# Kernel optimization log

Measured on AMD Instinct MI355X. Metric: run time of the kernel, lower is better.

The kernel has to match this reference:

```python
import jax, jax.numpy as jnp
import numpy as np

HEADS = 16
EMBED = 1024
D_K = EMBED // HEADS


def setup_inputs() -> dict:
    key = jax.random.key(0)
    ks = jax.random.split(key, 11)
    B, S, E = 4, 2048, EMBED
    sc = 0.02
    return {
        "query": jax.random.normal(ks[0], (B, S, E), jnp.float32),
        "key_": jax.random.normal(ks[1], (B, S, E), jnp.float32),
        "value": jax.random.normal(ks[2], (B, S, E), jnp.float32),
        "Wq": jax.random.normal(ks[3], (E, E), jnp.float32) * sc,
        "bq": jnp.zeros((E,), jnp.float32),
        "Wk": jax.random.normal(ks[4], (E, E), jnp.float32) * sc,
        "bk": jnp.zeros((E,), jnp.float32),
        "Wv": jax.random.normal(ks[5], (E, E), jnp.float32) * sc,
        "bv": jnp.zeros((E,), jnp.float32),
        "Wo": jax.random.normal(ks[6], (E, D_K), jnp.float32) * sc,  # out: Linear(heads*d_k -> d_k)
        "bo": jnp.zeros((D_K,), jnp.float32),
    }


def reference(query, key_, value, Wq, bq, Wk, bk, Wv, bv, Wo, bo):
    B, S, E = query.shape
    H, Dk = HEADS, D_K
    # QKV projections
    q = query @ Wq + bq          # (B,S,E)
    k = key_ @ Wk + bk
    v = value @ Wv + bv
    # split heads -> (B,H,S,Dk)
    q = q.reshape(B, S, H, Dk).transpose(0, 2, 1, 3)
    k = k.reshape(B, S, H, Dk).transpose(0, 2, 1, 3)
    v = v.reshape(B, S, H, Dk).transpose(0, 2, 1, 3)
    # attention: softmax(QK^T / sqrt(d_k)) V
    scores = jnp.einsum("bhqd,bhkd->bhqk", q, k) / jnp.sqrt(jnp.asarray(Dk, q.dtype))
    attn = jax.nn.softmax(scores, axis=-1)
    ctx = jnp.einsum("bhqk,bhkd->bhqd", attn, v)
    ctx = ctx.transpose(0, 2, 1, 3).reshape(B, S, E)
    # output projection (E -> d_k, as in source)
    return ctx @ Wo + bo
```

## Files before the change

kernel.cpp:

```cpp
#include <hip/hip_runtime.h>
#include <hip/hip_bf16.h>
#include <cstdint>
#include <cstddef>

#define DEVI static __device__ __forceinline__

typedef unsigned short u16;
typedef unsigned int u32;
typedef __bf16 bf16_t;
typedef __bf16 bf16x8 __attribute__((ext_vector_type(8)));
typedef float f32x4 __attribute__((ext_vector_type(4)));
typedef float f32x16 __attribute__((ext_vector_type(16)));

union U16x8 { uint4 u; bf16x8 v; };
union PU { u32 w[4]; bf16x8 v; };

#define QSCALE 0.1803368801111204f

DEVI void gload_lds16(const void* g, void* l) {
  __builtin_amdgcn_global_load_lds((const __attribute__((address_space(1))) void*)g,
                                   (__attribute__((address_space(3))) void*)l, 16, 0, 0);
}
DEVI void wait_vmcnt0() { asm volatile("s_waitcnt vmcnt(0)" ::: "memory"); }

DEVI u32 cvt_pk_bf16(float lo, float hi) {
  u32 r;
  asm("v_cvt_pk_bf16_f32 %0, %1, %2" : "=v"(r) : "v"(lo), "v"(hi));
  return r;
}

DEVI void permswap(u32& a, u32& b) {
  asm("v_permlane32_swap_b32 %0, %1" : "+v"(a), "+v"(b));
}

DEVI f32x16 mfma32(bf16x8 a, bf16x8 b, f32x16 c) {
  return __builtin_amdgcn_mfma_f32_32x32x16_bf16(a, b, c, 0, 0, 0);
}

DEVI bf16x8 lds_frag(const char* base, int row, int koff, int swz) {
  U16x8 u;
  u.u = *(const uint4*)(base + row * 128 + (koff ^ swz));
  return u.v;
}

__global__ __launch_bounds__(256) void k_transpose_convert(
    const float* __restrict__ src, bf16_t* __restrict__ dst, int R, int C, float scale) {
  int tiles_c = C >> 6;
  int tc = blockIdx.x % tiles_c;
  int tr = blockIdx.x / tiles_c;
  int r0 = tr << 6, c0 = tc << 6;
  __shared__ u16 tile[64][65];
  int t = threadIdx.x;
  #pragma unroll
  for (int p = 0; p < 4; ++p) {
    int idx = t + p * 256;
    int i = idx >> 4, j4 = (idx & 15) * 4;
    float4 f = *(const float4*)(src + (size_t)(r0 + i) * C + c0 + j4);
    tile[i][j4 + 0] = __builtin_bit_cast(u16, (bf16_t)(f.x * scale));
    tile[i][j4 + 1] = __builtin_bit_cast(u16, (bf16_t)(f.y * scale));
    tile[i][j4 + 2] = __builtin_bit_cast(u16, (bf16_t)(f.z * scale));
    tile[i][j4 + 3] = __builtin_bit_cast(u16, (bf16_t)(f.w * scale));
  }
  __syncthreads();
  #pragma unroll
  for (int p = 0; p < 2; ++p) {
    int idx = t + p * 256;
    int j = idx >> 3, i0 = (idx & 7) * 8;
    u16 us[8];
    #pragma unroll
    for (int e = 0; e < 8; ++e) us[e] = tile[i0 + e][j];
    uint4 o;
    o.x = (u32)us[0] | ((u32)us[1] << 16);
    o.y = (u32)us[2] | ((u32)us[3] << 16);
    o.z = (u32)us[4] | ((u32)us[5] << 16);
    o.w = (u32)us[6] | ((u32)us[7] << 16);
    *(uint4*)((u16*)dst + (size_t)(c0 + j) * R + r0 + i0) = o;
  }
}

__global__ __launch_bounds__(256) void k_proj_gemm(
    const float* __restrict__ Aq, const float* __restrict__ Ak, const float* __restrict__ Av,
    const bf16_t* __restrict__ WqT, const bf16_t* __restrict__ WkT, const bf16_t* __restrict__ WvT,
    const float* __restrict__ bq, const float* __restrict__ bk, const float* __restrict__ bv,
    bf16_t* __restrict__ qh, bf16_t* __restrict__ kh, bf16_t* __restrict__ vh) {
  int bx = blockIdx.x;
  int which = bx >> 9;
  int tt = bx & 511;
  int tile_m = tt & 63;
  int tile_n = tt >> 6;
  const float* A    = which == 0 ? Aq : which == 1 ? Ak : Av;
  const bf16_t* WT  = which == 0 ? WqT : which == 1 ? WkT : WvT;
  const float* bias = which == 0 ? bq : which == 1 ? bk : bv;
  const float bscale = which == 0 ? QSCALE : 1.0f;
  bf16_t* dst       = which == 0 ? qh : which == 1 ? kh : vh;

  const int t = threadIdx.x;
  const int l = t & 63;
  const int w = t >> 6;
  const int wm = w >> 1, wn = w & 1;
  const int c = l & 15, g = l >> 4;
  const int row0 = tile_m << 7;
  const int n0 = tile_n << 7;

  __shared__ __align__(16) char As[128 * 64 * 2];
  __shared__ __align__(16) char Bs[128 * 64 * 2];

  f32x4 acc[4][4];
  #pragma unroll
  for (int i = 0; i < 4; ++i)
    #pragma unroll
    for (int j = 0; j < 4; ++j) acc[i][j] = (f32x4){0.f, 0.f, 0.f, 0.f};

  const int arow_b = t >> 4, ac4 = t & 15;
  const int aswz = arow_b & 7;
  const float* agbase = A + (size_t)(row0 + arow_b) * 1024 + ac4 * 4;
  char* aldst = As + arow_b * 128 + (((ac4 >> 1) ^ aswz) << 4) + (ac4 & 1) * 8;

  for (int kt = 0; kt < 16; ++kt) {
    __syncthreads();
    {
      const float* ap = agbase + kt * 64;
      #pragma unroll
      for (int p = 0; p < 8; ++p) {
        float4 f = *(const float4*)(ap + (size_t)p * 16384);
        uint2 o;
        o.x = cvt_pk_bf16(f.x, f.y);
        o.y = cvt_pk_bf16(f.z, f.w);
        *(uint2*)(aldst + p * 2048) = o;
      }
    }
    #pragma unroll
    for (int cc = 0; cc < 4; ++cc) {
      int slot = w * 256 + cc * 64 + l;
      int row = slot >> 3, chs = slot & 7;
      const bf16_t* src = WT + (size_t)(n0 + row) * 1024 + kt * 64 + ((chs ^ (row & 7)) << 3);
      gload_lds16(src, Bs + (w * 256 + cc * 64) * 16);
    }
    wait_vmcnt0();
    __syncthreads();
    #pragma unroll
    for (int kk = 0; kk < 2; ++kk) {
      bf16x8 af[4], bfr[4];
      #pragma unroll
      for (int mi = 0; mi < 4; ++mi) {
        int row = wm * 64 + mi * 16 + c;
        U16x8 u; u.u = *(const uint4*)(As + row * 128 + ((kk * 64 + g * 16) ^ ((c & 7) << 4)));
        af[mi] = u.v;
      }
      #pragma unroll
      for (int ni = 0; ni < 4; ++ni) {
        int row = wn * 64 + ni * 16 + c;
        U16x8 u; u.u = *(const uint4*)(Bs + row * 128 + ((kk * 64 + g * 16) ^ ((c & 7) << 4)));
        bfr[ni] = u.v;
      }
      #pragma unroll
      for (int mi = 0; mi < 4; ++mi)
        #pragma unroll
        for (int ni = 0; ni < 4; ++ni)
          acc[mi][ni] = __builtin_amdgcn_mfma_f32_16x16x32_bf16(af[mi], bfr[ni], acc[mi][ni], 0, 0, 0);
    }
  }
  u16* dd = (u16*)dst;
  #pragma unroll
  for (int ni = 0; ni < 4; ++ni) {
    int col = n0 + wn * 64 + ni * 16 + c;
    float bb = bias[col] * bscale;
    int h = col >> 6, d = col & 63;
    #pragma unroll
    for (int mi = 0; mi < 4; ++mi) {
      #pragma unroll
      for (int r = 0; r < 4; ++r) {
        int rowg = row0 + wm * 64 + mi * 16 + g * 4 + r;
        int b = rowg >> 11, s = rowg & 2047;
        float vv = acc[mi][ni][r] + bb;
        size_t idx = (((size_t)b * 16 + h) * 2048 + s) * 64 + d;
        dd[idx] = __builtin_bit_cast(u16, (bf16_t)vv);
      }
    }
  }
}

__global__ __launch_bounds__(256) void k_transpose_v(
    const bf16_t* __restrict__ vh, bf16_t* __restrict__ vT) {
  int bh = blockIdx.x >> 5, st = blockIdx.x & 31;
  int s0 = st << 6;
  __shared__ __align__(16) u16 tile[64][72];
  int t = threadIdx.x;
  const u16* src = (const u16*)vh + ((size_t)bh * 2048 + s0) * 64;
  #pragma unroll
  for (int p = 0; p < 2; ++p) {
    int idx = t + p * 256;
    int s = idx >> 3, d0 = (idx & 7) * 8;
    uint4 v = *(const uint4*)(src + s * 64 + d0);
    *(uint4*)(&tile[s][d0]) = v;
  }
  __syncthreads();
  u16* dst = (u16*)vT + (size_t)bh * 64 * 2048 + s0;
  #pragma unroll
  for (int p = 0; p < 2; ++p) {
    int idx = t + p * 256;
    int d = idx >> 3, s1 = (idx & 7) * 8;
    u16 us[8];
    #pragma unroll
    for (int e = 0; e < 8; ++e) us[e] = tile[s1 + e][d];
    uint4 o;
    o.x = (u32)us[0] | ((u32)us[1] << 16);
    o.y = (u32)us[2] | ((u32)us[3] << 16);
    o.z = (u32)us[4] | ((u32)us[5] << 16);
    o.w = (u32)us[6] | ((u32)us[7] << 16);
    *(uint4*)(dst + (size_t)d * 2048 + s1) = o;
  }
}

__global__ __launch_bounds__(256, 4) void k_attn(
    const bf16_t* __restrict__ qh, const bf16_t* __restrict__ kh,
    const bf16_t* __restrict__ vT, bf16_t* __restrict__ ctx) {
  const int bid = blockIdx.x;
  const int bx = ((bid & 7) << 7) | (bid >> 3);
  const int bh = bx >> 4;
  const int qt = bx & 15;
  const int q0 = qt << 7;
  const int t = threadIdx.x, l = t & 63, w = t >> 6;
  const int q = l & 31;
  const int hi = l >> 5;
  const int swz = (q & 7) << 4;

  __shared__ __align__(16) char Ks[2][64 * 128];
  __shared__ __align__(16) char Vs[2][64 * 128];
  __shared__ __align__(16) float Dn[4][32];

  const u16* qrow = (const u16*)qh + ((size_t)bh * 2048 + q0 + w * 32 + q) * 64;
  bf16x8 qf0, qf1, qf2, qf3;
  {
    U16x8 u;
    u.u = *(const uint4*)(qrow + 0 * 16 + hi * 8); qf0 = u.v;
    u.u = *(const uint4*)(qrow + 1 * 16 + hi * 8); qf1 = u.v;
    u.u = *(const uint4*)(qrow + 2 * 16 + hi * 8); qf2 = u.v;
    u.u = *(const uint4*)(qrow + 3 * 16 + hi * 8); qf3 = u.v;
  }

  const f32x16 z16 = {0.f,0.f,0.f,0.f, 0.f,0.f,0.f,0.f, 0.f,0.f,0.f,0.f, 0.f,0.f,0.f,0.f};
  f32x16 oc0 = z16, oc1 = z16;
  float l_run = 0.f;

  const u16* kbh = (const u16*)kh + (size_t)bh * 2048 * 64;
  const u16* vbh = (const u16*)vT + (size_t)bh * 64 * 2048;

  auto stage = [&](int kvi, int buf) {
    int kbase = kvi << 6;
    #pragma unroll
    for (int cc = 0; cc < 2; ++cc) {
      int slot = w * 128 + cc * 64 + l;
      int row = slot >> 3, chs = slot & 7;
      gload_lds16(kbh + (size_t)(kbase + row) * 64 + ((chs ^ (row & 7)) << 3),
                  Ks[buf] + (w * 128 + cc * 64) * 16);
      gload_lds16(vbh + (size_t)row * 2048 + kbase + ((chs ^ (row & 7)) << 3),
                  Vs[buf] + (w * 128 + cc * 64) * 16);
    }
  };

  stage(0, 0);
  wait_vmcnt0();
  __syncthreads();

  for (int kv = 0; kv < 32; ++kv) {
    const int cur = kv & 1;
    if (kv < 31) stage(kv + 1, cur ^ 1);
    const char* Kc = Ks[cur];
    const char* Vc = Vs[cur];

    #pragma unroll
    for (int tt = 0; tt < 2; ++tt) {
      const int arow = tt * 32 + q;
      f32x16 st = z16;
      __builtin_amdgcn_s_setprio(1);
      st = mfma32(lds_frag(Kc, arow, 0 * 32 + hi * 16, swz), qf0, st);
      st = mfma32(lds_frag(Kc, arow, 1 * 32 + hi * 16, swz), qf1, st);
      st = mfma32(lds_frag(Kc, arow, 2 * 32 + hi * 16, swz), qf2, st);
      st = mfma32(lds_frag(Kc, arow, 3 * 32 + hi * 16, swz), qf3, st);
      __builtin_amdgcn_s_setprio(0);

      float e[16];
      #pragma unroll
      for (int i = 0; i < 16; ++i) {
        e[i] = __builtin_amdgcn_exp2f(st[i]);
        l_run += e[i];
      }

      #pragma unroll
      for (int cc = 0; cc < 2; ++cc) {
        u32 a  = cvt_pk_bf16(e[8 * cc + 0], e[8 * cc + 1]);
        u32 b  = cvt_pk_bf16(e[8 * cc + 4], e[8 * cc + 5]);
        u32 c2 = cvt_pk_bf16(e[8 * cc + 2], e[8 * cc + 3]);
        u32 d  = cvt_pk_bf16(e[8 * cc + 6], e[8 * cc + 7]);
        permswap(a, b);
        permswap(c2, d);
        PU pu;
        pu.w[0] = a; pu.w[1] = c2; pu.w[2] = b; pu.w[3] = d;
        const int ks = tt * 2 + cc;
        __builtin_amdgcn_s_setprio(1);
        oc0 = mfma32(pu.v, lds_frag(Vc, q,      ks * 32 + hi * 16, swz), oc0);
        oc1 = mfma32(pu.v, lds_frag(Vc, 32 + q, ks * 32 + hi * 16, swz), oc1);
        __builtin_amdgcn_s_setprio(0);
      }
    }
    wait_vmcnt0();
    __syncthreads();
  }

  l_run += __shfl_xor(l_run, 32);
  Dn[w][q] = 1.f / l_run;
  __syncthreads();

  const int b = bh >> 4, hh = bh & 15;
  u16* cb = (u16*)ctx;
  #pragma unroll
  for (int qd = 0; qd < 4; ++qd) {
    float4 dv = *(const float4*)&Dn[w][qd * 8 + hi * 4];
    #pragma unroll
    for (int r = 0; r < 4; ++r) {
      float inv = (&dv.x)[r];
      int qrow_g = q0 + w * 32 + qd * 8 + hi * 4 + r;
      size_t base = ((size_t)b * 2048 + qrow_g) * 1024 + hh * 64;
      float v0 = oc0[qd * 4 + r] * inv;
      float v1 = oc1[qd * 4 + r] * inv;
      cb[base + q]      = __builtin_bit_cast(u16, (bf16_t)v0);
      cb[base + 32 + q] = __builtin_bit_cast(u16, (bf16_t)v1);
    }
  }
}

__global__ __launch_bounds__(256) void k_out_gemm(
    const bf16_t* __restrict__ ctx, const bf16_t* __restrict__ WoT,
    const float* __restrict__ bo, float* __restrict__ out) {
  int tile_m = blockIdx.x;
  const int t = threadIdx.x, l = t & 63, w = t >> 6;
  const int wm = w >> 1, wn = w & 1;
  const int c = l & 15, g = l >> 4;
  const int row0 = tile_m << 7;

  __shared__ __align__(16) char As[128 * 64 * 2];
  __shared__ __align__(16) char Bs[64 * 64 * 2];

  f32x4 acc[4][2];
  #pragma unroll
  for (int i = 0; i < 4; ++i)
    #pragma unroll
    for (int j = 0; j < 2; ++j) acc[i][j] = (f32x4){0.f, 0.f, 0.f, 0.f};

  for (int kt = 0; kt < 16; ++kt) {
    __syncthreads();
    #pragma unroll
    for (int cc = 0; cc < 4; ++cc) {
      int slot = w * 256 + cc * 64 + l;
      int row = slot >> 3, chs = slot & 7;
      const bf16_t* src = ctx + (size_t)(row0 + row) * 1024 + kt * 64 + ((chs ^ (row & 7)) << 3);
      gload_lds16(src, As + (w * 256 + cc * 64) * 16);
    }
    #pragma unroll
    for (int cc = 0; cc < 2; ++cc) {
      int slot = w * 128 + cc * 64 + l;
      int row = slot >> 3, chs = slot & 7;
      const bf16_t* src = WoT + (size_t)row * 1024 + kt * 64 + ((chs ^ (row & 7)) << 3);
      gload_lds16(src, Bs + (w * 128 + cc * 64) * 16);
    }
    wait_vmcnt0();
    __syncthreads();
    #pragma unroll
    for (int kk = 0; kk < 2; ++kk) {
      bf16x8 af[4], bfr[2];
      #pragma unroll
      for (int mi = 0; mi < 4; ++mi) {
        int row = wm * 64 + mi * 16 + c;
        U16x8 u; u.u = *(const uint4*)(As + row * 128 + ((kk * 64 + g * 16) ^ ((c & 7) << 4)));
        af[mi] = u.v;
      }
      #pragma unroll
      for (int ni = 0; ni < 2; ++ni) {
        int row = wn * 32 + ni * 16 + c;
        U16x8 u; u.u = *(const uint4*)(Bs + row * 128 + ((kk * 64 + g * 16) ^ ((c & 7) << 4)));
        bfr[ni] = u.v;
      }
      #pragma unroll
      for (int mi = 0; mi < 4; ++mi)
        #pragma unroll
        for (int ni = 0; ni < 2; ++ni)
          acc[mi][ni] = __builtin_amdgcn_mfma_f32_16x16x32_bf16(af[mi], bfr[ni], acc[mi][ni], 0, 0, 0);
    }
  }
  #pragma unroll
  for (int ni = 0; ni < 2; ++ni) {
    int col = wn * 32 + ni * 16 + c;
    float bb = bo[col];
    #pragma unroll
    for (int mi = 0; mi < 4; ++mi) {
      #pragma unroll
      for (int r = 0; r < 4; ++r) {
        int rowg = row0 + wm * 64 + mi * 16 + g * 4 + r;
        out[(size_t)rowg * 64 + col] = acc[mi][ni][r] + bb;
      }
    }
  }
}

extern "C" void kernel_launch(void* const* d_in, const int* in_sizes, int n_in,
                              void* d_out, int out_size, void* d_ws, size_t ws_size,
                              hipStream_t stream) {
  (void)in_sizes; (void)n_in; (void)out_size; (void)ws_size;
  const float* query = (const float*)d_in[0];
  const float* key_  = (const float*)d_in[1];
  const float* value = (const float*)d_in[2];
  const float* Wq = (const float*)d_in[3];
  const float* bq = (const float*)d_in[4];
  const float* Wk = (const float*)d_in[5];
  const float* bk = (const float*)d_in[6];
  const float* Wv = (const float*)d_in[7];
  const float* bv = (const float*)d_in[8];
  const float* Wo = (const float*)d_in[9];
  const float* bo = (const float*)d_in[10];
  float* out = (float*)d_out;

  char* ws = (char*)d_ws;
  bf16_t* WqT = (bf16_t*)(ws + (size_t)0);
  bf16_t* WkT = (bf16_t*)(ws + ((size_t)2 << 20));
  bf16_t* WvT = (bf16_t*)(ws + ((size_t)4 << 20));
  bf16_t* WoT = (bf16_t*)(ws + ((size_t)6 << 20));
  bf16_t* qhd = (bf16_t*)(ws + ((size_t)8 << 20));
  bf16_t* khd = (bf16_t*)(ws + ((size_t)24 << 20));
  bf16_t* vhd = (bf16_t*)(ws + ((size_t)40 << 20));
  bf16_t* vT  = (bf16_t*)(ws + ((size_t)56 << 20));
  bf16_t* ctx = (bf16_t*)(ws + ((size_t)72 << 20));

  k_transpose_convert<<<256, 256, 0, stream>>>(Wq, WqT, 1024, 1024, QSCALE);
  k_transpose_convert<<<256, 256, 0, stream>>>(Wk, WkT, 1024, 1024, 1.0f);
  k_transpose_convert<<<256, 256, 0, stream>>>(Wv, WvT, 1024, 1024, 1.0f);
  k_transpose_convert<<<16, 256, 0, stream>>>(Wo, WoT, 1024, 64, 1.0f);

  k_proj_gemm<<<1536, 256, 0, stream>>>(query, key_, value, WqT, WkT, WvT,
                                        bq, bk, bv, qhd, khd, vhd);
  k_transpose_v<<<2048, 256, 0, stream>>>(vhd, vT);
  k_attn<<<1024, 256, 0, stream>>>(qhd, khd, vT, ctx);
  k_out_gemm<<<64, 256, 0, stream>>>(ctx, WoT, bo, out);
}
```

Baseline: 208.8 us.

## Register-prefetch next K tile in projection GEMM and remap tiles per XCD

The projection GEMM now loads the next K-slice of A and B into registers while the current slice is computed, replacing the synchronous global-to-LDS load plus wait each iteration. The B operand switches from direct global_load_lds to register staging. Block indices are also remapped so consecutive blocks on the same XCD share M tiles, which should improve L2 reuse. This roughly doubles the register footprint for staged tiles and could reduce occupancy.

```diff
diff --git a/kernel.cpp b/kernel.cpp
--- a/kernel.cpp
+++ b/kernel.cpp
@@ -83,11 +83,12 @@
     const bf16_t* __restrict__ WqT, const bf16_t* __restrict__ WkT, const bf16_t* __restrict__ WvT,
     const float* __restrict__ bq, const float* __restrict__ bk, const float* __restrict__ bv,
     bf16_t* __restrict__ qh, bf16_t* __restrict__ kh, bf16_t* __restrict__ vh) {
-  int bx = blockIdx.x;
-  int which = bx >> 9;
-  int tt = bx & 511;
-  int tile_m = tt & 63;
-  int tile_n = tt >> 6;
+  const int bid = blockIdx.x;
+  const int which = bid >> 9;
+  const int b9 = bid & 511;
+  const int xcd = b9 & 7, j = b9 >> 3;
+  const int tile_m = xcd * 8 + (j >> 3);
+  const int tile_n = j & 7;
   const float* A    = which == 0 ? Aq : which == 1 ? Ak : Av;
   const bf16_t* WT  = which == 0 ? WqT : which == 1 ? WkT : WvT;
   const float* bias = which == 0 ? bq : which == 1 ? bk : bv;
@@ -109,35 +110,43 @@
   #pragma unroll
   for (int i = 0; i < 4; ++i)
     #pragma unroll
-    for (int j = 0; j < 4; ++j) acc[i][j] = (f32x4){0.f, 0.f, 0.f, 0.f};
+    for (int jj = 0; jj < 4; ++jj) acc[i][jj] = (f32x4){0.f, 0.f, 0.f, 0.f};
 
   const int arow_b = t >> 4, ac4 = t & 15;
-  const int aswz = arow_b & 7;
   const float* agbase = A + (size_t)(row0 + arow_b) * 1024 + ac4 * 4;
-  char* aldst = As + arow_b * 128 + (((ac4 >> 1) ^ aswz) << 4) + (ac4 & 1) * 8;
-
-  for (int kt = 0; kt < 16; ++kt) {
-    __syncthreads();
-    {
-      const float* ap = agbase + kt * 64;
-      #pragma unroll
-      for (int p = 0; p < 8; ++p) {
-        float4 f = *(const float4*)(ap + (size_t)p * 16384);
-        uint2 o;
-        o.x = cvt_pk_bf16(f.x, f.y);
-        o.y = cvt_pk_bf16(f.z, f.w);
-        *(uint2*)(aldst + p * 2048) = o;
-      }
-    }
-    #pragma unroll
-    for (int cc = 0; cc < 4; ++cc) {
-      int slot = w * 256 + cc * 64 + l;
-      int row = slot >> 3, chs = slot & 7;
-      const bf16_t* src = WT + (size_t)(n0 + row) * 1024 + kt * 64 + ((chs ^ (row & 7)) << 3);
-      gload_lds16(src, Bs + (w * 256 + cc * 64) * 16);
-    }
-    wait_vmcnt0();
-    __syncthreads();
+  char* aldst = As + arow_b * 128 + (((ac4 >> 1) ^ (arow_b & 7)) << 4) + (ac4 & 1) * 8;
+
+  const int brow_b = t >> 3, bchs = t & 7;
+  const u16* bgbase = (const u16*)WT + (size_t)(n0 + brow_b) * 1024 + bchs * 8;
+  char* bldst = Bs + brow_b * 128 + ((bchs ^ (brow_b & 7)) << 4);
+
+  float4 fa0[8], fa1[8];
+  uint4 fb0[4], fb1[4];
+
+  auto loadA = [&](int kt, float4* f) {
+    const float* ap = agbase + kt * 64;
+    #pragma unroll
+    for (int p = 0; p < 8; ++p) f[p] = *(const float4*)(ap + (size_t)p * 16384);
+  };
+  auto loadB = [&](int kt, uint4* u) {
+    const u16* bp = bgbase + kt * 64;
+    #pragma unroll
+    for (int p = 0; p < 4; ++p) u[p] = *(const uint4*)(bp + (size_t)p * 32768);
+  };
+  auto storeA = [&](const float4* f) {
+    #pragma unroll
+    for (int p = 0; p < 8; ++p) {
+      uint2 o;
+      o.x = cvt_pk_bf16(f[p].x, f[p].y);
+      o.y = cvt_pk_bf16(f[p].z, f[p].w);
+      *(uint2*)(aldst + p * 2048) = o;
+    }
+  };
+  auto storeB = [&](const uint4* u) {
+    #pragma unroll
+    for (int p = 0; p < 4; ++p) *(uint4*)(bldst + p * 4096) = u[p];
+  };
+  auto compute = [&]() {
     #pragma unroll
     for (int kk = 0; kk < 2; ++kk) {
       bf16x8 af[4], bfr[4];
@@ -159,7 +168,22 @@
         for (int ni = 0; ni < 4; ++ni)
           acc[mi][ni] = __builtin_amdgcn_mfma_f32_16x16x32_bf16(af[mi], bfr[ni], acc[mi][ni], 0, 0, 0);
     }
-  }
+  };
+
+  loadA(0, fa0); loadB(0, fb0);
+  for (int i = 0; i < 8; ++i) {
+    __syncthreads();
+    storeA(fa0); storeB(fb0);
+    loadA(2 * i + 1, fa1); loadB(2 * i + 1, fb1);
+    __syncthreads();
+    compute();
+    __syncthreads();
+    storeA(fa1); storeB(fb1);
+    if (i < 7) { loadA(2 * i + 2, fa0); loadB(2 * i + 2, fb0); }
+    __syncthreads();
+    compute();
+  }
+
   u16* dd = (u16*)dst;
   #pragma unroll
   for (int ni = 0; ni < 4; ++ni) {
```

Result: slower. 286.7 us (+37.3%).

## Prefetch next K-tile into registers to overlap global loads with MFMA

Applied to the files above, without the earlier changes.

Restructures the QKV projection GEMM main loop so that the A (fp32) and B (bf16 weight) tiles for the next K step are loaded into registers while the current tile's MFMAs run, then converted and stored to LDS after a barrier. The weight tile now goes through registers instead of the direct global-to-LDS load path. This hides global memory latency behind compute, at the cost of more live registers (around 48 extra VGPRs for the prefetch buffers), which may lower occupancy.

```diff
diff --git a/kernel.cpp b/kernel.cpp
--- a/kernel.cpp
+++ b/kernel.cpp
@@ -83,11 +83,11 @@
     const bf16_t* __restrict__ WqT, const bf16_t* __restrict__ WkT, const bf16_t* __restrict__ WvT,
     const float* __restrict__ bq, const float* __restrict__ bk, const float* __restrict__ bv,
     bf16_t* __restrict__ qh, bf16_t* __restrict__ kh, bf16_t* __restrict__ vh) {
-  int bx = blockIdx.x;
-  int which = bx >> 9;
-  int tt = bx & 511;
-  int tile_m = tt & 63;
-  int tile_n = tt >> 6;
+  const int bx = blockIdx.x;
+  const int which = bx >> 9;
+  const int tt = bx & 511;
+  const int tile_m = tt & 63;
+  const int tile_n = tt >> 6;
   const float* A    = which == 0 ? Aq : which == 1 ? Ak : Av;
   const bf16_t* WT  = which == 0 ? WqT : which == 1 ? WkT : WvT;
   const float* bias = which == 0 ? bq : which == 1 ? bk : bv;
@@ -112,32 +112,40 @@
     for (int j = 0; j < 4; ++j) acc[i][j] = (f32x4){0.f, 0.f, 0.f, 0.f};
 
   const int arow_b = t >> 4, ac4 = t & 15;
-  const int aswz = arow_b & 7;
   const float* agbase = A + (size_t)(row0 + arow_b) * 1024 + ac4 * 4;
-  char* aldst = As + arow_b * 128 + (((ac4 >> 1) ^ aswz) << 4) + (ac4 & 1) * 8;
+  char* aldst = As + arow_b * 128 + (((ac4 >> 1) ^ (arow_b & 7)) << 4) + (ac4 & 1) * 8;
+
+  const int brow_b = t >> 3, bchs = t & 7;
+  const u16* bgbase = (const u16*)WT + (size_t)(n0 + brow_b) * 1024 + bchs * 8;
+  char* bldst = Bs + brow_b * 128 + ((bchs ^ (brow_b & 7)) << 4);
+
+  float4 fa[8];
+  uint4 fb[4];
+
+  #pragma unroll
+  for (int p = 0; p < 8; ++p) fa[p] = *(const float4*)(agbase + (size_t)p * 16384);
+  #pragma unroll
+  for (int p = 0; p < 4; ++p) fb[p] = *(const uint4*)(bgbase + (size_t)p * 32768);
+  #pragma unroll
+  for (int p = 0; p < 8; ++p) {
+    uint2 o;
+    o.x = cvt_pk_bf16(fa[p].x, fa[p].y);
+    o.y = cvt_pk_bf16(fa[p].z, fa[p].w);
+    *(uint2*)(aldst + p * 2048) = o;
+  }
+  #pragma unroll
+  for (int p = 0; p < 4; ++p) *(uint4*)(bldst + p * 4096) = fb[p];
+  __syncthreads();
 
   for (int kt = 0; kt < 16; ++kt) {
-    __syncthreads();
-    {
-      const float* ap = agbase + kt * 64;
-      #pragma unroll
-      for (int p = 0; p < 8; ++p) {
-        float4 f = *(const float4*)(ap + (size_t)p * 16384);
-        uint2 o;
-        o.x = cvt_pk_bf16(f.x, f.y);
-        o.y = cvt_pk_bf16(f.z, f.w);
-        *(uint2*)(aldst + p * 2048) = o;
-      }
-    }
-    #pragma unroll
-    for (int cc = 0; cc < 4; ++cc) {
-      int slot = w * 256 + cc * 64 + l;
-      int row = slot >> 3, chs = slot & 7;
-      const bf16_t* src = WT + (size_t)(n0 + row) * 1024 + kt * 64 + ((chs ^ (row & 7)) << 3);
-      gload_lds16(src, Bs + (w * 256 + cc * 64) * 16);
-    }
-    wait_vmcnt0();
-    __syncthreads();
+    if (kt < 15) {
+      const float* ap = agbase + (kt + 1) * 64;
+      #pragma unroll
+      for (int p = 0; p < 8; ++p) fa[p] = *(const float4*)(ap + (size_t)p * 16384);
+      const u16* bp = bgbase + (kt + 1) * 64;
+      #pragma unroll
+      for (int p = 0; p < 4; ++p) fb[p] = *(const uint4*)(bp + (size_t)p * 32768);
+    }
     #pragma unroll
     for (int kk = 0; kk < 2; ++kk) {
       bf16x8 af[4], bfr[4];
@@ -159,7 +167,21 @@
         for (int ni = 0; ni < 4; ++ni)
           acc[mi][ni] = __builtin_amdgcn_mfma_f32_16x16x32_bf16(af[mi], bfr[ni], acc[mi][ni], 0, 0, 0);
     }
-  }
+    __syncthreads();
+    if (kt < 15) {
+      #pragma unroll
+      for (int p = 0; p < 8; ++p) {
+        uint2 o;
+        o.x = cvt_pk_bf16(fa[p].x, fa[p].y);
+        o.y = cvt_pk_bf16(fa[p].z, fa[p].w);
+        *(uint2*)(aldst + p * 2048) = o;
+      }
+      #pragma unroll
+      for (int p = 0; p < 4; ++p) *(uint4*)(bldst + p * 4096) = fb[p];
+      __syncthreads();
+    }
+  }
+
   u16* dd = (u16*)dst;
   #pragma unroll
   for (int ni = 0; ni < 4; ++ni) {
```

After: 262.3 us. 25.6% more time.

## Pre-convert fp32 activations to bf16 and stream A tiles via direct LDS loads

Applied to the files above, without the earlier changes.

Adds a separate kernel that converts query, key and value from fp32 to bf16 into workspace. When the workspace is large enough, the projection GEMM then loads A tiles with global_load_lds, the same way it loads the weights. This replaces the per-k-step fp32 register loads and in-kernel conversion, and it halves the bytes each of the 8 N-tiles rereads. The cost is an extra kernel launch plus a full read and write of about 48M elements, and the path is gated on the workspace size.

```diff
diff --git a/kernel.cpp b/kernel.cpp
--- a/kernel.cpp
+++ b/kernel.cpp
@@ -23,6 +23,12 @@
 }
 DEVI void wait_vmcnt0() { asm volatile("s_waitcnt vmcnt(0)" ::: "memory"); }
 
+DEVI u32 pack2(float a, float b) {
+  u16 x = __builtin_bit_cast(u16, (bf16_t)a);
+  u16 y = __builtin_bit_cast(u16, (bf16_t)b);
+  return (u32)x | ((u32)y << 16);
+}
+
 DEVI u32 cvt_pk_bf16(float lo, float hi) {
   u32 r;
   asm("v_cvt_pk_bf16_f32 %0, %1, %2" : "=v"(r) : "v"(lo), "v"(hi));
@@ -41,6 +47,26 @@
   U16x8 u;
   u.u = *(const uint4*)(base + row * 128 + (koff ^ swz));
   return u.v;
+}
+
+__global__ __launch_bounds__(256) void k_cvt3(
+    const float* __restrict__ a, const float* __restrict__ b, const float* __restrict__ c,
+    bf16_t* __restrict__ dst) {
+  int which = blockIdx.x >> 10;
+  int bb = blockIdx.x & 1023;
+  const float* s = which == 0 ? a : which == 1 ? b : c;
+  u16* d = (u16*)dst + (size_t)which * 8192 * 1024;
+  size_t base = ((size_t)bb * 256 + threadIdx.x) * 8;
+  #pragma unroll
+  for (int p = 0; p < 4; ++p) {
+    size_t i = base + (size_t)p * 2097152;
+    float4 f0 = *(const float4*)(s + i);
+    float4 f1 = *(const float4*)(s + i + 4);
+    uint4 o;
+    o.x = cvt_pk_bf16(f0.x, f0.y); o.y = cvt_pk_bf16(f0.z, f0.w);
+    o.z = cvt_pk_bf16(f1.x, f1.y); o.w = cvt_pk_bf16(f1.z, f1.w);
+    *(uint4*)(d + i) = o;
+  }
 }
 
 __global__ __launch_bounds__(256) void k_transpose_convert(
@@ -78,8 +104,10 @@
   }
 }
 
+template<bool PRE>
 __global__ __launch_bounds__(256) void k_proj_gemm(
     const float* __restrict__ Aq, const float* __restrict__ Ak, const float* __restrict__ Av,
+    const bf16_t* __restrict__ Abf,
     const bf16_t* __restrict__ WqT, const bf16_t* __restrict__ WkT, const bf16_t* __restrict__ WvT,
     const float* __restrict__ bq, const float* __restrict__ bk, const float* __restrict__ bv,
     bf16_t* __restrict__ qh, bf16_t* __restrict__ kh, bf16_t* __restrict__ vh) {
@@ -89,6 +117,7 @@
   int tile_m = tt & 63;
   int tile_n = tt >> 6;
   const float* A    = which == 0 ? Aq : which == 1 ? Ak : Av;
+  const bf16_t* Ab  = Abf + (size_t)which * 8192 * 1024;
   const bf16_t* WT  = which == 0 ? WqT : which == 1 ? WkT : WvT;
   const float* bias = which == 0 ? bq : which == 1 ? bk : bv;
   const float bscale = which == 0 ? QSCALE : 1.0f;
@@ -112,13 +141,20 @@
     for (int j = 0; j < 4; ++j) acc[i][j] = (f32x4){0.f, 0.f, 0.f, 0.f};
 
   const int arow_b = t >> 4, ac4 = t & 15;
-  const int aswz = arow_b & 7;
   const float* agbase = A + (size_t)(row0 + arow_b) * 1024 + ac4 * 4;
-  char* aldst = As + arow_b * 128 + (((ac4 >> 1) ^ aswz) << 4) + (ac4 & 1) * 8;
+  char* aldst = As + arow_b * 128 + (((ac4 >> 1) ^ (arow_b & 7)) << 4) + (ac4 & 1) * 8;
 
   for (int kt = 0; kt < 16; ++kt) {
     __syncthreads();
-    {
+    if constexpr (PRE) {
+      #pragma unroll
+      for (int cc = 0; cc < 4; ++cc) {
+        int slot = w * 256 + cc * 64 + l;
+        int row = slot >> 3, chs = slot & 7;
+        const bf16_t* src = Ab + (size_t)(row0 + row) * 1024 + kt * 64 + ((chs ^ (row & 7)) << 3);
+        gload_lds16(src, As + (w * 256 + cc * 64) * 16);
+      }
+    } else {
       const float* ap = agbase + kt * 64;
       #pragma unroll
       for (int p = 0; p < 8; ++p) {
@@ -406,7 +442,7 @@
 extern "C" void kernel_launch(void* const* d_in, const int* in_sizes, int n_in,
                               void* d_out, int out_size, void* d_ws, size_t ws_size,
                               hipStream_t stream) {
-  (void)in_sizes; (void)n_in; (void)out_size; (void)ws_size;
+  (void)in_sizes; (void)n_in; (void)out_size;
   const float* query = (const float*)d_in[0];
   const float* key_  = (const float*)d_in[1];
   const float* value = (const float*)d_in[2];
@@ -430,14 +466,23 @@
   bf16_t* vhd = (bf16_t*)(ws + ((size_t)40 << 20));
   bf16_t* vT  = (bf16_t*)(ws + ((size_t)56 << 20));
   bf16_t* ctx = (bf16_t*)(ws + ((size_t)72 << 20));
+  bf16_t* Abf = (bf16_t*)(ws + ((size_t)88 << 20));
+
+  const bool pre = ws_size >= ((size_t)137 << 20);
 
   k_transpose_convert<<<256, 256, 0, stream>>>(Wq, WqT, 1024, 1024, QSCALE);
   k_transpose_convert<<<256, 256, 0, stream>>>(Wk, WkT, 1024, 1024, 1.0f);
   k_transpose_convert<<<256, 256, 0, stream>>>(Wv, WvT, 1024, 1024, 1.0f);
   k_transpose_convert<<<16, 256, 0, stream>>>(Wo, WoT, 1024, 64, 1.0f);
 
-  k_proj_gemm<<<1536, 256, 0, stream>>>(query, key_, value, WqT, WkT, WvT,
-                                        bq, bk, bv, qhd, khd, vhd);
+  if (pre) {
+    k_cvt3<<<3072, 256, 0, stream>>>(query, key_, value, Abf);
+    k_proj_gemm<true><<<1536, 256, 0, stream>>>(query, key_, value, Abf, WqT, WkT, WvT,
+                                                bq, bk, bv, qhd, khd, vhd);
+  } else {
+    k_proj_gemm<false><<<1536, 256, 0, stream>>>(query, key_, value, Abf, WqT, WkT, WvT,
+                                                 bq, bk, bv, qhd, khd, vhd);
+  }
   k_transpose_v<<<2048, 256, 0, stream>>>(vhd, vT);
   k_attn<<<1024, 256, 0, stream>>>(qhd, khd, vT, ctx);
   k_out_gemm<<<64, 256, 0, stream>>>(ctx, WoT, bo, out);
```

Measured after the change: 204.7 us. -2.0%, faster.
